# Kernel optimization log

Measured on AMD Instinct MI355X. Metric: run time of the kernel, lower is better.

The kernel has to match this reference:

```python
import jax, jax.numpy as jnp
import numpy as np

HEADS_FEAT = 8
HEADS_SAMP = 8
EPS = 1e-5


def _ln(x, g, b):
    m = jnp.mean(x, -1, keepdims=True)
    v = jnp.mean((x - m) ** 2, -1, keepdims=True)
    return (x - m) * jax.lax.rsqrt(v + EPS) * g + b


def _mha(q, k, v, heads, Wq, bq, Wk, bk, Wv, bv, Wo, bo, bias=None):
    # q: (N, Lq, D), k/v: (N, Lk, D); torch nn.MultiheadAttention math (eval, dropout=0)
    N, Lq, D = q.shape
    Lk = k.shape[1]
    dh = D // heads
    qh = (jnp.einsum('nld,ed->nle', q, Wq) + bq).reshape(N, Lq, heads, dh).transpose(0, 2, 1, 3)
    kh = (jnp.einsum('nld,ed->nle', k, Wk) + bk).reshape(N, Lk, heads, dh).transpose(0, 2, 1, 3)
    vh = (jnp.einsum('nld,ed->nle', v, Wv) + bv).reshape(N, Lk, heads, dh).transpose(0, 2, 1, 3)
    s = jnp.einsum('nhqd,nhkd->nhqk', qh, kh) * (dh ** -0.5)
    if bias is not None:
        s = s + bias  # bias broadcasts over heads
    a = jax.nn.softmax(s, axis=-1)
    o = jnp.einsum('nhqk,nhkd->nhqd', a, vh).transpose(0, 2, 1, 3).reshape(N, Lq, D)
    return jnp.einsum('nld,ed->nle', o, Wo) + bo


def setup_inputs() -> dict:
    key = jax.random.key(0)
    B, S, F, D = 4, 512, 32, 256
    H = 4 * D
    ks = iter(jax.random.split(key, 64))
    p = {}
    p['x'] = jax.random.normal(next(ks), (B, S, F, D), jnp.float32)
    m = jax.random.bernoulli(next(ks), 0.5, (B, F, F))
    p['attn_mask'] = m | jnp.eye(F, dtype=bool)  # diagonal True avoids fully-masked rows
    p['N_train'] = 384
    p['N_test'] = 128
    def W(shape):
        return jax.random.normal(next(ks), shape, jnp.float32) * 0.02
    for sfx in ('f', 't', 's'):
        for nm in ('Wq', 'Wk', 'Wv', 'Wo'):
            p[nm + '_' + sfx] = W((D, D))
        for nm in ('bq', 'bk', 'bv', 'bo'):
            p[nm + '_' + sfx] = jnp.zeros((D,), jnp.float32)
    for sfx in ('f', 't', 's', 'm'):
        p['g_' + sfx] = jnp.ones((D,), jnp.float32)
        p['b_' + sfx] = jnp.zeros((D,), jnp.float32)
    p['W1'] = W((H, D)); p['b1'] = jnp.zeros((H,), jnp.float32)
    p['Wg'] = W((H, D)); p['bg'] = jnp.zeros((H,), jnp.float32)
    p['W2'] = W((D, H)); p['b2'] = jnp.zeros((D,), jnp.float32)
    return p


def reference(x, attn_mask, N_train, N_test,
              Wq_f, bq_f, Wk_f, bk_f, Wv_f, bv_f, Wo_f, bo_f,
              Wq_t, bq_t, Wk_t, bk_t, Wv_t, bv_t, Wo_t, bo_t,
              Wq_s, bq_s, Wk_s, bk_s, Wv_s, bv_s, Wo_s, bo_s,
              g_f, b_f, g_t, b_t, g_s, b_s, g_m, b_m,
              W1, b1, Wg, bg, W2, b2):
    B, S, F, D = x.shape
    # --- graph-masked feature attention over F (rows = B*S) ---
    x_row = x.reshape(B * S, F, D)
    x_norm = _ln(x_row, g_f, b_f)
    bias = jnp.where(attn_mask, 0.0, -jnp.inf).astype(x.dtype)  # (B,F,F)
    bias = jnp.broadcast_to(bias[:, None, None], (B, S, 1, F, F)).reshape(B * S, 1, F, F)
    x2 = _mha(x_norm, x_norm, x_norm, HEADS_FEAT, Wq_f, bq_f, Wk_f, bk_f, Wv_f, bv_f, Wo_f, bo_f, bias)
    x_row = x_row + x2
    # --- sample attention over S (columns = B*F) ---
    x_col = x_row.reshape(B, S, F, D).transpose(0, 2, 1, 3).reshape(B * F, S, D)
    x_tr = x_col[:, :N_train]
    x_te = x_col[:, N_train:]
    x_trn = _ln(x_tr, g_t, b_t)
    x_tr = x_tr + _mha(x_trn, x_trn, x_trn, HEADS_SAMP, Wq_t, bq_t, Wk_t, bk_t, Wv_t, bv_t, Wo_t, bo_t)
    if N_test > 0:
        x_ten = _ln(x_te, g_s, b_s)
        kvn = _ln(x_tr, g_s, b_s)
        x_te = x_te + _mha(x_ten, kvn, kvn, HEADS_SAMP, Wq_s, bq_s, Wk_s, bk_s, Wv_s, bv_s, Wo_s, bo_s)
    xc = jnp.concatenate([x_tr, x_te], axis=1).reshape(B, F, S, D).transpose(0, 2, 1, 3)
    # --- SwiGLU MLP ---
    xn = _ln(xc, g_m, b_m)
    h = (jnp.einsum('bsfd,ed->bsfe', xn, W1) + b1) * jax.nn.silu(jnp.einsum('bsfd,ed->bsfe', xn, Wg) + bg)
    x2 = jnp.einsum('bsfe,de->bsfd', h, W2) + b2
    return xc + x2
```

## Files before the change

kernel.cpp:

```cpp
#include <hip/hip_runtime.h>

typedef unsigned short u16;
typedef __attribute__((ext_vector_type(8))) short short8;
typedef __attribute__((ext_vector_type(4))) float f32x4;

#define SCALE_QK 0.17677669529663687f
#define LOG2E 1.44269504088896f

__device__ __forceinline__ u16 f2b(float f) {
  union { float f; unsigned int i; } v; v.f = f;
  unsigned int x = v.i;
  x += 0x7fffu + ((x >> 16) & 1u);
  return (u16)(x >> 16);
}
__device__ __forceinline__ float lo16(unsigned int u) {
  union { unsigned int i; float f; } v; v.i = u << 16; return v.f;
}
__device__ __forceinline__ float hi16(unsigned int u) {
  union { unsigned int i; float f; } v; v.i = u & 0xffff0000u; return v.f;
}

__device__ __forceinline__ size_t map_off(int m, int map) {
  if (map == 0) return ((size_t)m) << 8;
  int r, s;
  if (map == 1) { r = m / 384; s = m - r * 384; }
  else          { r = m >> 7;  s = 384 + (m & 127); }
  int b = r >> 5, f = r & 31;
  return ((size_t)((b * 512 + s) * 32 + f)) << 8;
}

__global__ void decode_mask_kernel(const int* __restrict__ mraw,
                                   float* __restrict__ bias) {
  __shared__ int isbyte;
  if (threadIdx.x == 0) isbyte = 0;
  __syncthreads();
  for (int i = threadIdx.x; i < 1024; i += 256) {
    unsigned int v = (unsigned int)mraw[i];
    if (v > 1u) atomicOr(&isbyte, 1);
  }
  __syncthreads();
  bool byt = (isbyte != 0);
  const unsigned char* mb = (const unsigned char*)mraw;
  for (int i = threadIdx.x; i < 4096; i += 256) {
    bool on = byt ? (mb[i] != 0) : (mraw[i] != 0);
    bias[i] = on ? 0.f : -1e30f;
  }
}

struct WPtrs { const float* p[15]; };
__global__ __launch_bounds__(256) void cvt_w_kernel(WPtrs wp, u16* __restrict__ out) {
  int gid = blockIdx.x * 256 + threadIdx.x;
  int e0 = gid * 8;
  if (e0 >= 1572864) return;
  int mi, off;
  if (e0 < 786432) { mi = e0 >> 16; off = e0 & 65535; }
  else { int j = e0 - 786432; mi = 12 + (j >> 18); off = j & 262143; }
  const float* s = wp.p[mi] + off;
  float4 a = *(const float4*)s;
  float4 b = *(const float4*)(s + 4);
  union { u16 u[8]; uint4 v; } pk;
  pk.u[0] = f2b(a.x); pk.u[1] = f2b(a.y); pk.u[2] = f2b(a.z); pk.u[3] = f2b(a.w);
  pk.u[4] = f2b(b.x); pk.u[5] = f2b(b.y); pk.u[6] = f2b(b.z); pk.u[7] = f2b(b.w);
  *(uint4*)(out + e0) = pk.v;
}

__global__ __launch_bounds__(256) void ln_kernel(
    const float* __restrict__ src, float* __restrict__ cpy,
    u16* __restrict__ dst, const float* __restrict__ g,
    const float* __restrict__ bt, int M, int map) {
  int widx = blockIdx.x * 4 + (threadIdx.x >> 6);
  if (widx >= M) return;
  int lane = threadIdx.x & 63;
  size_t off = map_off(widx, map);
  float4 xv = ((const float4*)(src + off))[lane];
  float s = xv.x + xv.y + xv.z + xv.w;
#pragma unroll
  for (int o = 32; o; o >>= 1) s += __shfl_xor(s, o);
  float mean = s * (1.f / 256.f);
  float dx = xv.x - mean, dy = xv.y - mean, dz = xv.z - mean, dw = xv.w - mean;
  float ss = dx * dx + dy * dy + dz * dz + dw * dw;
#pragma unroll
  for (int o = 32; o; o >>= 1) ss += __shfl_xor(ss, o);
  float rs = rsqrtf(ss * (1.f / 256.f) + 1e-5f);
  float4 gv = ((const float4*)g)[lane];
  float4 bv = ((const float4*)bt)[lane];
  ushort4 st;
  st.x = f2b(dx * rs * gv.x + bv.x);
  st.y = f2b(dy * rs * gv.y + bv.y);
  st.z = f2b(dz * rs * gv.z + bv.z);
  st.w = f2b(dw * rs * gv.w + bv.w);
  *(ushort4*)(dst + ((size_t)widx << 8) + lane * 4) = st;
  if (cpy) ((float4*)(cpy + off))[lane] = xv;
}

__global__ __launch_bounds__(256) void gemm_nt(
    const u16* __restrict__ A, const u16* __restrict__ W,
    const float* __restrict__ bias, u16* __restrict__ outB,
    float* __restrict__ outF, int M, int N, int K, int mode) {
  __shared__ u16 As[2 * 64 * 32];
  __shared__ u16 Ws[2 * 64 * 32];
  int tid = threadIdx.x, lane = tid & 63, w = tid >> 6;
  int wr = w >> 1, wc = w & 1;
  int m0 = blockIdx.x * 64, n0 = blockIdx.y * 64;
  f32x4 z = {0.f, 0.f, 0.f, 0.f};
  f32x4 acc[2][2];
  acc[0][0] = z; acc[0][1] = z; acc[1][0] = z; acc[1][1] = z;
  int r = tid >> 2;
  int segbase = (tid & 3) << 1;
  for (int kt = 0; kt < K; kt += 64) {
#pragma unroll
    for (int c = 0; c < 2; ++c) {
      int seg = segbase + c;
      int dsti = (seg >> 2) * 2048 + r * 32 + (seg & 3) * 8;
      *(uint4*)&As[dsti] = *(const uint4*)(A + (size_t)(m0 + r) * K + kt + seg * 8);
      *(uint4*)&Ws[dsti] = *(const uint4*)(W + (size_t)(n0 + r) * K + kt + seg * 8);
    }
    __syncthreads();
#pragma unroll
    for (int ks = 0; ks < 2; ++ks) {
      const u16* ab = As + ks * 2048 + (lane & 15) * 32 + (lane >> 4) * 8;
      const u16* bb = Ws + ks * 2048 + (lane & 15) * 32 + (lane >> 4) * 8;
      short8 a0 = *(const short8*)(ab + (wr * 32) * 32);
      short8 a1 = *(const short8*)(ab + (wr * 32 + 16) * 32);
      short8 b0 = *(const short8*)(bb + (wc * 32) * 32);
      short8 b1 = *(const short8*)(bb + (wc * 32 + 16) * 32);
      acc[0][0] = __builtin_amdgcn_mfma_f32_16x16x32_bf16(a0, b0, acc[0][0], 0, 0, 0);
      acc[0][1] = __builtin_amdgcn_mfma_f32_16x16x32_bf16(a0, b1, acc[0][1], 0, 0, 0);
      acc[1][0] = __builtin_amdgcn_mfma_f32_16x16x32_bf16(a1, b0, acc[1][0], 0, 0, 0);
      acc[1][1] = __builtin_amdgcn_mfma_f32_16x16x32_bf16(a1, b1, acc[1][1], 0, 0, 0);
    }
    __syncthreads();
  }
  int ln_ = lane & 15, lg = lane >> 4;
#pragma unroll
  for (int mi = 0; mi < 2; ++mi)
#pragma unroll
    for (int ni = 0; ni < 2; ++ni) {
      int col = n0 + wc * 32 + ni * 16 + ln_;
      float bv = bias ? bias[col] : 0.f;
#pragma unroll
      for (int rr = 0; rr < 4; ++rr) {
        int row = m0 + wr * 32 + mi * 16 + lg * 4 + rr;
        float v = acc[mi][ni][rr] + bv;
        if (mode == 0) {
          outB[(size_t)row * N + col] = f2b(v);
        } else {
          size_t off = map_off(row, mode - 1) + col;
          outF[off] += v;
        }
      }
    }
}

__global__ __launch_bounds__(256) void gemm_dual(
    const u16* __restrict__ A, const u16* __restrict__ W1,
    const float* __restrict__ b1, const u16* __restrict__ Wg,
    const float* __restrict__ bg, u16* __restrict__ Hb,
    int M, int N, int K) {
  __shared__ u16 As[2 * 64 * 32];
  __shared__ u16 W1s[2 * 64 * 32];
  __shared__ u16 Wgs[2 * 64 * 32];
  int tid = threadIdx.x, lane = tid & 63, w = tid >> 6;
  int wr = w >> 1, wc = w & 1;
  int m0 = blockIdx.x * 64, n0 = blockIdx.y * 64;
  f32x4 z = {0.f, 0.f, 0.f, 0.f};
  f32x4 ac1[2][2], ac2[2][2];
  ac1[0][0] = z; ac1[0][1] = z; ac1[1][0] = z; ac1[1][1] = z;
  ac2[0][0] = z; ac2[0][1] = z; ac2[1][0] = z; ac2[1][1] = z;
  int r = tid >> 2;
  int segbase = (tid & 3) << 1;
  for (int kt = 0; kt < K; kt += 64) {
#pragma unroll
    for (int c = 0; c < 2; ++c) {
      int seg = segbase + c;
      int dsti = (seg >> 2) * 2048 + r * 32 + (seg & 3) * 8;
      *(uint4*)&As[dsti]  = *(const uint4*)(A  + (size_t)(m0 + r) * K + kt + seg * 8);
      *(uint4*)&W1s[dsti] = *(const uint4*)(W1 + (size_t)(n0 + r) * K + kt + seg * 8);
      *(uint4*)&Wgs[dsti] = *(const uint4*)(Wg + (size_t)(n0 + r) * K + kt + seg * 8);
    }
    __syncthreads();
#pragma unroll
    for (int ks = 0; ks < 2; ++ks) {
      const u16* ab = As + ks * 2048 + (lane & 15) * 32 + (lane >> 4) * 8;
      const u16* b1b = W1s + ks * 2048 + (lane & 15) * 32 + (lane >> 4) * 8;
      const u16* b2b = Wgs + ks * 2048 + (lane & 15) * 32 + (lane >> 4) * 8;
      short8 a0 = *(const short8*)(ab + (wr * 32) * 32);
      short8 a1 = *(const short8*)(ab + (wr * 32 + 16) * 32);
      short8 p0 = *(const short8*)(b1b + (wc * 32) * 32);
      short8 p1 = *(const short8*)(b1b + (wc * 32 + 16) * 32);
      short8 q0 = *(const short8*)(b2b + (wc * 32) * 32);
      short8 q1 = *(const short8*)(b2b + (wc * 32 + 16) * 32);
      ac1[0][0] = __builtin_amdgcn_mfma_f32_16x16x32_bf16(a0, p0, ac1[0][0], 0, 0, 0);
      ac1[0][1] = __builtin_amdgcn_mfma_f32_16x16x32_bf16(a0, p1, ac1[0][1], 0, 0, 0);
      ac1[1][0] = __builtin_amdgcn_mfma_f32_16x16x32_bf16(a1, p0, ac1[1][0], 0, 0, 0);
      ac1[1][1] = __builtin_amdgcn_mfma_f32_16x16x32_bf16(a1, p1, ac1[1][1], 0, 0, 0);
      ac2[0][0] = __builtin_amdgcn_mfma_f32_16x16x32_bf16(a0, q0, ac2[0][0], 0, 0, 0);
      ac2[0][1] = __builtin_amdgcn_mfma_f32_16x16x32_bf16(a0, q1, ac2[0][1], 0, 0, 0);
      ac2[1][0] = __builtin_amdgcn_mfma_f32_16x16x32_bf16(a1, q0, ac2[1][0], 0, 0, 0);
      ac2[1][1] = __builtin_amdgcn_mfma_f32_16x16x32_bf16(a1, q1, ac2[1][1], 0, 0, 0);
    }
    __syncthreads();
  }
  int ln_ = lane & 15, lg = lane >> 4;
#pragma unroll
  for (int mi = 0; mi < 2; ++mi)
#pragma unroll
    for (int ni = 0; ni < 2; ++ni) {
      int col = n0 + wc * 32 + ni * 16 + ln_;
      float bb1 = b1[col], bbg = bg[col];
#pragma unroll
      for (int rr = 0; rr < 4; ++rr) {
        int row = m0 + wr * 32 + mi * 16 + lg * 4 + rr;
        float v1 = ac1[mi][ni][rr] + bb1;
        float v2 = ac2[mi][ni][rr] + bbg;
        float sg = v2 / (1.f + __expf(-v2));
        Hb[(size_t)row * N + col] = f2b(v1 * sg);
      }
    }
}

__global__ __launch_bounds__(256) void fa_kernel(
    const u16* __restrict__ Q, const u16* __restrict__ K,
    const u16* __restrict__ V, u16* __restrict__ CTX,
    const float* __restrict__ bias) {
  __shared__ u16 Ks[8192];
  __shared__ u16 Vs[8192];
  __shared__ float Bs[1056];
  int tid = threadIdx.x;
  int row = blockIdx.x;
  size_t base = (size_t)row << 13;
#pragma unroll
  for (int it = 0; it < 4; ++it) {
    int c = it * 256 + tid;
    int tok = c >> 5, d8 = c & 31;
    int dst = ((d8 >> 2) * 32 + tok) * 32 + (d8 & 3) * 8;
    *(uint4*)&Ks[dst] = *(const uint4*)(K + base + tok * 256 + d8 * 8);
    *(uint4*)&Vs[dst] = *(const uint4*)(V + base + tok * 256 + d8 * 8);
  }
  {
    const float* bp = bias + (size_t)(row >> 9) * 1024;
#pragma unroll
    for (int it = 0; it < 4; ++it) {
      int i = it * 256 + tid;
      Bs[(i >> 5) * 33 + (i & 31)] = bp[i];
    }
  }
  __syncthreads();
  int h = tid >> 5, q = tid & 31;
  float qr[32];
  {
    const u16* qp = Q + base + q * 256 + h * 32;
    const float sc = SCALE_QK * LOG2E;
#pragma unroll
    for (int j = 0; j < 4; ++j) {
      uint4 u = ((const uint4*)qp)[j];
      qr[j * 8 + 0] = lo16(u.x) * sc; qr[j * 8 + 1] = hi16(u.x) * sc;
      qr[j * 8 + 2] = lo16(u.y) * sc; qr[j * 8 + 3] = hi16(u.y) * sc;
      qr[j * 8 + 4] = lo16(u.z) * sc; qr[j * 8 + 5] = hi16(u.z) * sc;
      qr[j * 8 + 6] = lo16(u.w) * sc; qr[j * 8 + 7] = hi16(u.w) * sc;
    }
  }
  float s[32], m = -3e38f;
  const u16* kb = Ks + h * 1024;
  const float* brow = Bs + q * 33;
#pragma unroll 4
  for (int k = 0; k < 32; ++k) {
    const uint4* kr = (const uint4*)(kb + k * 32);
    float d0 = 0.f, d1 = 0.f, d2 = 0.f, d3 = 0.f;
#pragma unroll
    for (int j = 0; j < 4; ++j) {
      uint4 u = kr[j];
      d0 += qr[j * 8 + 0] * lo16(u.x); d1 += qr[j * 8 + 1] * hi16(u.x);
      d2 += qr[j * 8 + 2] * lo16(u.y); d3 += qr[j * 8 + 3] * hi16(u.y);
      d0 += qr[j * 8 + 4] * lo16(u.z); d1 += qr[j * 8 + 5] * hi16(u.z);
      d2 += qr[j * 8 + 6] * lo16(u.w); d3 += qr[j * 8 + 7] * hi16(u.w);
    }
    float sv = (d0 + d1) + (d2 + d3) + brow[k];
    s[k] = sv;
    m = fmaxf(m, sv);
  }
  float l = 0.f;
#pragma unroll
  for (int k = 0; k < 32; ++k) {
    float p = exp2f(s[k] - m);
    s[k] = p; l += p;
  }
  float inv = 1.f / l;
  float out[32];
#pragma unroll
  for (int d = 0; d < 32; ++d) out[d] = 0.f;
  const u16* vb = Vs + h * 1024;
#pragma unroll 4
  for (int k = 0; k < 32; ++k) {
    float wgt = s[k];
    const uint4* vr = (const uint4*)(vb + k * 32);
#pragma unroll
    for (int j = 0; j < 4; ++j) {
      uint4 u = vr[j];
      out[j * 8 + 0] += wgt * lo16(u.x); out[j * 8 + 1] += wgt * hi16(u.x);
      out[j * 8 + 2] += wgt * lo16(u.y); out[j * 8 + 3] += wgt * hi16(u.y);
      out[j * 8 + 4] += wgt * lo16(u.z); out[j * 8 + 5] += wgt * hi16(u.z);
      out[j * 8 + 6] += wgt * lo16(u.w); out[j * 8 + 7] += wgt * hi16(u.w);
    }
  }
  u16* op = CTX + base + q * 256 + h * 32;
#pragma unroll
  for (int j = 0; j < 4; ++j) {
    union { u16 u[8]; uint4 v; } pk;
#pragma unroll
    for (int e = 0; e < 8; ++e) pk.u[e] = f2b(out[j * 8 + e] * inv);
    ((uint4*)op)[j] = pk.v;
  }
}

__global__ __launch_bounds__(256) void sa_mfma_kernel(
    const u16* __restrict__ Q, const u16* __restrict__ K,
    const u16* __restrict__ V, u16* __restrict__ CTX, int Lq) {
  __shared__ u16 Ks[384 * 40];
  __shared__ u16 Vt[32 * 392];
  __shared__ u16 Pb[4][16 * 72];
  int tid = threadIdx.x, lane = tid & 63, w = tid >> 6;
  int rh = blockIdx.x;
  int row = rh >> 3, h = rh & 7;
  size_t kvb = ((size_t)row * 384) * 256 + h * 32;
  for (int c = tid; c < 1536; c += 256) {
    int k = c >> 2, seg = c & 3;
    uint4 kk = *(const uint4*)(K + kvb + (size_t)k * 256 + seg * 8);
    *(uint4*)&Ks[k * 40 + seg * 8] = kk;
    uint4 vv = *(const uint4*)(V + kvb + (size_t)k * 256 + seg * 8);
    union { u16 u[8]; uint4 v; } t; t.v = vv;
#pragma unroll
    for (int j = 0; j < 8; ++j) Vt[(seg * 8 + j) * 392 + k] = t.u[j];
  }
  __syncthreads();
  int fr = lane & 15, fg = lane >> 4;
  const float sc = SCALE_QK * LOG2E;
  int nqt = Lq >> 4;
  f32x4 zz = {0.f, 0.f, 0.f, 0.f};
  for (int qt = w; qt < nqt; qt += 4) {
    int q0 = qt << 4;
    short8 a_q = *(const short8*)(Q + ((size_t)row * Lq + q0 + fr) * 256 + h * 32 + fg * 8);
    f32x4 O0 = zz, O1 = zz;
    float m[4] = {-3e38f, -3e38f, -3e38f, -3e38f};
    float l[4] = {0.f, 0.f, 0.f, 0.f};
    u16* pb = Pb[w];
    for (int c0 = 0; c0 < 384; c0 += 64) {
      f32x4 s[4];
#pragma unroll
      for (int kt = 0; kt < 4; ++kt) {
        short8 b_k = *(const short8*)(Ks + (c0 + kt * 16 + fr) * 40 + fg * 8);
        s[kt] = __builtin_amdgcn_mfma_f32_16x16x32_bf16(a_q, b_k, zz, 0, 0, 0);
      }
      float rm[4];
#pragma unroll
      for (int r = 0; r < 4; ++r)
        rm[r] = fmaxf(fmaxf(s[0][r], s[1][r]), fmaxf(s[2][r], s[3][r]));
#pragma unroll
      for (int o = 1; o <= 8; o <<= 1)
#pragma unroll
        for (int r = 0; r < 4; ++r) rm[r] = fmaxf(rm[r], __shfl_xor(rm[r], o));
      float al[4];
#pragma unroll
      for (int r = 0; r < 4; ++r) {
        float mn = fmaxf(m[r], rm[r] * sc);
        al[r] = exp2f(m[r] - mn);
        m[r] = mn;
        l[r] *= al[r];
        O0[r] *= al[r];
        O1[r] *= al[r];
      }
#pragma unroll
      for (int kt = 0; kt < 4; ++kt)
#pragma unroll
        for (int r = 0; r < 4; ++r) {
          float p = exp2f(fmaf(s[kt][r], sc, -m[r]));
          l[r] += p;
          pb[(fg * 4 + r) * 72 + kt * 16 + fr] = f2b(p);
        }
      asm volatile("s_waitcnt lgkmcnt(0)" ::: "memory");
      __builtin_amdgcn_wave_barrier();
#pragma unroll
      for (int sub = 0; sub < 2; ++sub) {
        short8 a_p = *(const short8*)(pb + fr * 72 + sub * 32 + fg * 8);
        short8 b_v0 = *(const short8*)(Vt + fr * 392 + c0 + sub * 32 + fg * 8);
        short8 b_v1 = *(const short8*)(Vt + (16 + fr) * 392 + c0 + sub * 32 + fg * 8);
        O0 = __builtin_amdgcn_mfma_f32_16x16x32_bf16(a_p, b_v0, O0, 0, 0, 0);
        O1 = __builtin_amdgcn_mfma_f32_16x16x32_bf16(a_p, b_v1, O1, 0, 0, 0);
      }
      __builtin_amdgcn_wave_barrier();
    }
#pragma unroll
    for (int o = 1; o <= 8; o <<= 1)
#pragma unroll
      for (int r = 0; r < 4; ++r) l[r] += __shfl_xor(l[r], o);
    u16* op = CTX + ((size_t)row * Lq + q0) * 256 + h * 32;
#pragma unroll
    for (int r = 0; r < 4; ++r) {
      float inv = 1.f / l[r];
      int orow = fg * 4 + r;
      op[orow * 256 + fr] = f2b(O0[r] * inv);
      op[orow * 256 + 16 + fr] = f2b(O1[r] * inv);
    }
  }
}

extern "C" void kernel_launch(void* const* d_in, const int* in_sizes, int n_in,
                              void* d_out, int out_size, void* d_ws, size_t ws_size,
                              hipStream_t stream) {
  const float* x    = (const float*)d_in[0];
  const int*   mask = (const int*)d_in[1];
  const float* bq_f = (const float*)d_in[8],  *bk_f = (const float*)d_in[9];
  const float* bv_f = (const float*)d_in[10], *bo_f = (const float*)d_in[11];
  const float* bq_t = (const float*)d_in[16], *bk_t = (const float*)d_in[17];
  const float* bv_t = (const float*)d_in[18], *bo_t = (const float*)d_in[19];
  const float* bq_s = (const float*)d_in[24], *bk_s = (const float*)d_in[25];
  const float* bv_s = (const float*)d_in[26], *bo_s = (const float*)d_in[27];
  const float* g_f = (const float*)d_in[28], *b_f = (const float*)d_in[29];
  const float* g_t = (const float*)d_in[30], *b_t = (const float*)d_in[31];
  const float* g_s = (const float*)d_in[32], *b_s = (const float*)d_in[33];
  const float* g_m = (const float*)d_in[34], *b_m = (const float*)d_in[35];
  const float* b1 = (const float*)d_in[37];
  const float* bg = (const float*)d_in[39];
  const float* b2 = (const float*)d_in[41];

  float* XR = (float*)d_out;
  char* ws = (char*)d_ws;
  float* BIAS = (float*)ws;
  u16* XN = (u16*)(ws + 16384);
  u16* QB = XN + 16777216;
  u16* KB = QB + 16777216;
  u16* VB = KB + 16777216;
  u16* XM = VB + 16777216;
  u16* WB = XM + 16777216;
  u16* HB = XN;

  WPtrs wp;
  wp.p[0] = (const float*)d_in[4];  wp.p[1] = (const float*)d_in[5];
  wp.p[2] = (const float*)d_in[6];  wp.p[3] = (const float*)d_in[7];
  wp.p[4] = (const float*)d_in[12]; wp.p[5] = (const float*)d_in[13];
  wp.p[6] = (const float*)d_in[14]; wp.p[7] = (const float*)d_in[15];
  wp.p[8] = (const float*)d_in[20]; wp.p[9] = (const float*)d_in[21];
  wp.p[10] = (const float*)d_in[22]; wp.p[11] = (const float*)d_in[23];
  wp.p[12] = (const float*)d_in[36]; wp.p[13] = (const float*)d_in[38];
  wp.p[14] = (const float*)d_in[40];
  const u16 *WQF = WB, *WKF = WB + 65536, *WVF = WB + 131072, *WOF = WB + 196608;
  const u16 *WQT = WB + 262144, *WKT = WB + 327680, *WVT = WB + 393216, *WOT = WB + 458752;
  const u16 *WQS = WB + 524288, *WKS = WB + 589824, *WVS = WB + 655360, *WOS = WB + 720896;
  const u16 *W1B = WB + 786432, *WGB = WB + 1048576, *W2B = WB + 1310720;

  cvt_w_kernel<<<768, 256, 0, stream>>>(wp, WB);
  decode_mask_kernel<<<1, 256, 0, stream>>>(mask, BIAS);

  ln_kernel<<<16384, 256, 0, stream>>>(x, XR, XN, g_f, b_f, 65536, 0);
  gemm_nt<<<dim3(1024, 4), 256, 0, stream>>>(XN, WQF, bq_f, QB, nullptr, 65536, 256, 256, 0);
  gemm_nt<<<dim3(1024, 4), 256, 0, stream>>>(XN, WKF, bk_f, KB, nullptr, 65536, 256, 256, 0);
  gemm_nt<<<dim3(1024, 4), 256, 0, stream>>>(XN, WVF, bv_f, VB, nullptr, 65536, 256, 256, 0);
  fa_kernel<<<2048, 256, 0, stream>>>(QB, KB, VB, XN, BIAS);
  gemm_nt<<<dim3(1024, 4), 256, 0, stream>>>(XN, WOF, bo_f, nullptr, XR, 65536, 256, 256, 1);

  ln_kernel<<<12288, 256, 0, stream>>>(XR, nullptr, XN, g_t, b_t, 49152, 1);
  gemm_nt<<<dim3(768, 4), 256, 0, stream>>>(XN, WQT, bq_t, QB, nullptr, 49152, 256, 256, 0);
  gemm_nt<<<dim3(768, 4), 256, 0, stream>>>(XN, WKT, bk_t, KB, nullptr, 49152, 256, 256, 0);
  gemm_nt<<<dim3(768, 4), 256, 0, stream>>>(XN, WVT, bv_t, VB, nullptr, 49152, 256, 256, 0);
  sa_mfma_kernel<<<1024, 256, 0, stream>>>(QB, KB, VB, XN, 384);
  gemm_nt<<<dim3(768, 4), 256, 0, stream>>>(XN, WOT, bo_t, nullptr, XR, 49152, 256, 256, 2);

  ln_kernel<<<4096, 256, 0, stream>>>(XR, nullptr, XN, g_s, b_s, 16384, 2);
  gemm_nt<<<dim3(256, 4), 256, 0, stream>>>(XN, WQS, bq_s, QB, nullptr, 16384, 256, 256, 0);
  ln_kernel<<<12288, 256, 0, stream>>>(XR, nullptr, XN, g_s, b_s, 49152, 1);
  gemm_nt<<<dim3(768, 4), 256, 0, stream>>>(XN, WKS, bk_s, KB, nullptr, 49152, 256, 256, 0);
  gemm_nt<<<dim3(768, 4), 256, 0, stream>>>(XN, WVS, bv_s, VB, nullptr, 49152, 256, 256, 0);
  sa_mfma_kernel<<<1024, 256, 0, stream>>>(QB, KB, VB, XN, 128);
  gemm_nt<<<dim3(256, 4), 256, 0, stream>>>(XN, WOS, bo_s, nullptr, XR, 16384, 256, 256, 3);

  ln_kernel<<<16384, 256, 0, stream>>>(XR, nullptr, XM, g_m, b_m, 65536, 0);
  gemm_dual<<<dim3(1024, 16), 256, 0, stream>>>(XM, W1B, b1, WGB, bg, HB, 65536, 1024, 256);
  gemm_nt<<<dim3(1024, 4), 256, 0, stream>>>(HB, W2B, b2, nullptr, XR, 65536, 256, 1024, 1);
}
```

Before: 975.7 us.

## Enlarge GEMM tiles to 128x128 and load tiles via direct global-to-LDS

Both GEMM kernels move from 64x64 to 128x128 output tiles with a 4x4 MFMA accumulator grid per wave, which raises operand reuse out of LDS and cuts redundant global reads. Tile staging now uses global_load_lds to copy straight into shared memory instead of going through registers. The catch is much higher register pressure, especially in gemm_dual with 32 accumulators, and unpadded 64-wide LDS rows that may cause bank conflicts. Launch grids are halved in each dimension to match.

```diff
diff --git a/kernel.cpp b/kernel.cpp
--- a/kernel.cpp
+++ b/kernel.cpp
@@ -18,6 +18,11 @@
 }
 __device__ __forceinline__ float hi16(unsigned int u) {
   union { unsigned int i; float f; } v; v.i = u & 0xffff0000u; return v.f;
+}
+__device__ __forceinline__ void gll16(const void* g, void* l) {
+  __builtin_amdgcn_global_load_lds(
+      (const __attribute__((address_space(1))) unsigned int*)g,
+      (__attribute__((address_space(3))) unsigned int*)l, 16, 0, 0);
 }
 
 __device__ __forceinline__ size_t map_off(int m, int map) {
@@ -93,126 +98,132 @@
   if (cpy) ((float4*)(cpy + off))[lane] = xv;
 }
 
-__global__ __launch_bounds__(256) void gemm_nt(
+__global__ __launch_bounds__(256, 2) void gemm_nt(
     const u16* __restrict__ A, const u16* __restrict__ W,
     const float* __restrict__ bias, u16* __restrict__ outB,
     float* __restrict__ outF, int M, int N, int K, int mode) {
-  __shared__ u16 As[2 * 64 * 32];
-  __shared__ u16 Ws[2 * 64 * 32];
+  __shared__ u16 As[128 * 64];
+  __shared__ u16 Bs[128 * 64];
   int tid = threadIdx.x, lane = tid & 63, w = tid >> 6;
   int wr = w >> 1, wc = w & 1;
-  int m0 = blockIdx.x * 64, n0 = blockIdx.y * 64;
+  int m0 = blockIdx.x * 128, n0 = blockIdx.y * 128;
+  int fr = lane & 15, fg = lane >> 4;
   f32x4 z = {0.f, 0.f, 0.f, 0.f};
-  f32x4 acc[2][2];
-  acc[0][0] = z; acc[0][1] = z; acc[1][0] = z; acc[1][1] = z;
-  int r = tid >> 2;
-  int segbase = (tid & 3) << 1;
+  f32x4 acc[4][4];
+#pragma unroll
+  for (int i = 0; i < 4; ++i)
+#pragma unroll
+    for (int j = 0; j < 4; ++j) acc[i][j] = z;
+  int r8 = lane >> 3, seg = lane & 7;
+  const u16* gA = A + (size_t)(m0 + w * 32 + r8) * K + seg * 8;
+  const u16* gB = W + (size_t)(n0 + w * 32 + r8) * K + seg * 8;
+  u16* lA = As + (w * 32) * 64;
+  u16* lB = Bs + (w * 32) * 64;
   for (int kt = 0; kt < K; kt += 64) {
 #pragma unroll
-    for (int c = 0; c < 2; ++c) {
-      int seg = segbase + c;
-      int dsti = (seg >> 2) * 2048 + r * 32 + (seg & 3) * 8;
-      *(uint4*)&As[dsti] = *(const uint4*)(A + (size_t)(m0 + r) * K + kt + seg * 8);
-      *(uint4*)&Ws[dsti] = *(const uint4*)(W + (size_t)(n0 + r) * K + kt + seg * 8);
+    for (int j = 0; j < 4; ++j) {
+      gll16(gA + (size_t)(j * 8) * K + kt, lA + j * 512);
+      gll16(gB + (size_t)(j * 8) * K + kt, lB + j * 512);
     }
     __syncthreads();
 #pragma unroll
     for (int ks = 0; ks < 2; ++ks) {
-      const u16* ab = As + ks * 2048 + (lane & 15) * 32 + (lane >> 4) * 8;
-      const u16* bb = Ws + ks * 2048 + (lane & 15) * 32 + (lane >> 4) * 8;
-      short8 a0 = *(const short8*)(ab + (wr * 32) * 32);
-      short8 a1 = *(const short8*)(ab + (wr * 32 + 16) * 32);
-      short8 b0 = *(const short8*)(bb + (wc * 32) * 32);
-      short8 b1 = *(const short8*)(bb + (wc * 32 + 16) * 32);
-      acc[0][0] = __builtin_amdgcn_mfma_f32_16x16x32_bf16(a0, b0, acc[0][0], 0, 0, 0);
-      acc[0][1] = __builtin_amdgcn_mfma_f32_16x16x32_bf16(a0, b1, acc[0][1], 0, 0, 0);
-      acc[1][0] = __builtin_amdgcn_mfma_f32_16x16x32_bf16(a1, b0, acc[1][0], 0, 0, 0);
-      acc[1][1] = __builtin_amdgcn_mfma_f32_16x16x32_bf16(a1, b1, acc[1][1], 0, 0, 0);
+      short8 af[4], bf[4];
+#pragma unroll
+      for (int i = 0; i < 4; ++i) {
+        af[i] = *(const short8*)(As + (wr * 64 + i * 16 + fr) * 64 + ks * 32 + fg * 8);
+        bf[i] = *(const short8*)(Bs + (wc * 64 + i * 16 + fr) * 64 + ks * 32 + fg * 8);
+      }
+#pragma unroll
+      for (int mi = 0; mi < 4; ++mi)
+#pragma unroll
+        for (int ni = 0; ni < 4; ++ni)
+          acc[mi][ni] = __builtin_amdgcn_mfma_f32_16x16x32_bf16(af[mi], bf[ni], acc[mi][ni], 0, 0, 0);
     }
     __syncthreads();
   }
-  int ln_ = lane & 15, lg = lane >> 4;
-#pragma unroll
-  for (int mi = 0; mi < 2; ++mi)
-#pragma unroll
-    for (int ni = 0; ni < 2; ++ni) {
-      int col = n0 + wc * 32 + ni * 16 + ln_;
+#pragma unroll
+  for (int mi = 0; mi < 4; ++mi)
+#pragma unroll
+    for (int ni = 0; ni < 4; ++ni) {
+      int col = n0 + wc * 64 + ni * 16 + fr;
       float bv = bias ? bias[col] : 0.f;
 #pragma unroll
-      for (int rr = 0; rr < 4; ++rr) {
-        int row = m0 + wr * 32 + mi * 16 + lg * 4 + rr;
-        float v = acc[mi][ni][rr] + bv;
+      for (int r = 0; r < 4; ++r) {
+        int row = m0 + wr * 64 + mi * 16 + fg * 4 + r;
+        float v = acc[mi][ni][r] + bv;
         if (mode == 0) {
           outB[(size_t)row * N + col] = f2b(v);
         } else {
-          size_t off = map_off(row, mode - 1) + col;
-          outF[off] += v;
+          outF[map_off(row, mode - 1) + col] += v;
         }
       }
     }
 }
 
-__global__ __launch_bounds__(256) void gemm_dual(
+__global__ __launch_bounds__(256, 2) void gemm_dual(
     const u16* __restrict__ A, const u16* __restrict__ W1,
     const float* __restrict__ b1, const u16* __restrict__ Wg,
     const float* __restrict__ bg, u16* __restrict__ Hb,
     int M, int N, int K) {
-  __shared__ u16 As[2 * 64 * 32];
-  __shared__ u16 W1s[2 * 64 * 32];
-  __shared__ u16 Wgs[2 * 64 * 32];
+  __shared__ u16 As[128 * 64];
+  __shared__ u16 W1s[128 * 64];
+  __shared__ u16 Wgs[128 * 64];
   int tid = threadIdx.x, lane = tid & 63, w = tid >> 6;
   int wr = w >> 1, wc = w & 1;
-  int m0 = blockIdx.x * 64, n0 = blockIdx.y * 64;
+  int m0 = blockIdx.x * 128, n0 = blockIdx.y * 128;
+  int fr = lane & 15, fg = lane >> 4;
   f32x4 z = {0.f, 0.f, 0.f, 0.f};
-  f32x4 ac1[2][2], ac2[2][2];
-  ac1[0][0] = z; ac1[0][1] = z; ac1[1][0] = z; ac1[1][1] = z;
-  ac2[0][0] = z; ac2[0][1] = z; ac2[1][0] = z; ac2[1][1] = z;
-  int r = tid >> 2;
-  int segbase = (tid & 3) << 1;
+  f32x4 ac1[4][4], ac2[4][4];
+#pragma unroll
+  for (int i = 0; i < 4; ++i)
+#pragma unroll
+    for (int j = 0; j < 4; ++j) { ac1[i][j] = z; ac2[i][j] = z; }
+  int r8 = lane >> 3, seg = lane & 7;
+  const u16* gA = A + (size_t)(m0 + w * 32 + r8) * K + seg * 8;
+  const u16* g1 = W1 + (size_t)(n0 + w * 32 + r8) * K + seg * 8;
+  const u16* g2 = Wg + (size_t)(n0 + w * 32 + r8) * K + seg * 8;
+  u16* lA = As + (w * 32) * 64;
+  u16* l1 = W1s + (w * 32) * 64;
+  u16* l2 = Wgs + (w * 32) * 64;
   for (int kt = 0; kt < K; kt += 64) {
 #pragma unroll
-    for (int c = 0; c < 2; ++c) {
-      int seg = segbase + c;
-      int dsti = (seg >> 2) * 2048 + r * 32 + (seg & 3) * 8;
-      *(uint4*)&As[dsti]  = *(const uint4*)(A  + (size_t)(m0 + r) * K + kt + seg * 8);
-      *(uint4*)&W1s[dsti] = *(const uint4*)(W1 + (size_t)(n0 + r) * K + kt + seg * 8);
-      *(uint4*)&Wgs[dsti] = *(const uint4*)(Wg + (size_t)(n0 + r) * K + kt + seg * 8);
+    for (int j = 0; j < 4; ++j) {
+      gll16(gA + (size_t)(j * 8) * K + kt, lA + j * 512);
+      gll16(g1 + (size_t)(j * 8) * K + kt, l1 + j * 512);
+      gll16(g2 + (size_t)(j * 8) * K + kt, l2 + j * 512);
     }
     __syncthreads();
 #pragma unroll
     for (int ks = 0; ks < 2; ++ks) {
-      const u16* ab = As + ks * 2048 + (lane & 15) * 32 + (lane >> 4) * 8;
-      const u16* b1b = W1s + ks * 2048 + (lane & 15) * 32 + (lane >> 4) * 8;
-      const u16* b2b = Wgs + ks * 2048 + (lane & 15) * 32 + (lane >> 4) * 8;
-      short8 a0 = *(const short8*)(ab + (wr * 32) * 32);
-      short8 a1 = *(const short8*)(ab + (wr * 32 + 16) * 32);
-      short8 p0 = *(const short8*)(b1b + (wc * 32) * 32);
-      short8 p1 = *(const short8*)(b1b + (wc * 32 + 16) * 32);
-      short8 q0 = *(const short8*)(b2b + (wc * 32) * 32);
-      short8 q1 = *(const short8*)(b2b + (wc * 32 + 16) * 32);
-      ac1[0][0] = __builtin_amdgcn_mfma_f32_16x16x32_bf16(a0, p0, ac1[0][0], 0, 0, 0);
-      ac1[0][1] = __builtin_amdgcn_mfma_f32_16x16x32_bf16(a0, p1, ac1[0][1], 0, 0, 0);
-      ac1[1][0] = __builtin_amdgcn_mfma_f32_16x16x32_bf16(a1, p0, ac1[1][0], 0, 0, 0);
-      ac1[1][1] = __builtin_amdgcn_mfma_f32_16x16x32_bf16(a1, p1, ac1[1][1], 0, 0, 0);
-      ac2[0][0] = __builtin_amdgcn_mfma_f32_16x16x32_bf16(a0, q0, ac2[0][0], 0, 0, 0);
-      ac2[0][1] = __builtin_amdgcn_mfma_f32_16x16x32_bf16(a0, q1, ac2[0][1], 0, 0, 0);
-      ac2[1][0] = __builtin_amdgcn_mfma_f32_16x16x32_bf16(a1, q0, ac2[1][0], 0, 0, 0);
-      ac2[1][1] = __builtin_amdgcn_mfma_f32_16x16x32_bf16(a1, q1, ac2[1][1], 0, 0, 0);
+      short8 af[4], bf1[4], bf2[4];
+#pragma unroll
+      for (int i = 0; i < 4; ++i) {
+        af[i]  = *(const short8*)(As  + (wr * 64 + i * 16 + fr) * 64 + ks * 32 + fg * 8);
+        bf1[i] = *(const short8*)(W1s + (wc * 64 + i * 16 + fr) * 64 + ks * 32 + fg * 8);
+        bf2[i] = *(const short8*)(Wgs + (wc * 64 + i * 16 + fr) * 64 + ks * 32 + fg * 8);
+      }
+#pragma unroll
+      for (int mi = 0; mi < 4; ++mi)
+#pragma unroll
+        for (int ni = 0; ni < 4; ++ni) {
+          ac1[mi][ni] = __builtin_amdgcn_mfma_f32_16x16x32_bf16(af[mi], bf1[ni], ac1[mi][ni], 0, 0, 0);
+          ac2[mi][ni] = __builtin_amdgcn_mfma_f32_16x16x32_bf16(af[mi], bf2[ni], ac2[mi][ni], 0, 0, 0);
+        }
     }
     __syncthreads();
   }
-  int ln_ = lane & 15, lg = lane >> 4;
-#pragma unroll
-  for (int mi = 0; mi < 2; ++mi)
-#pragma unroll
-    for (int ni = 0; ni < 2; ++ni) {
-      int col = n0 + wc * 32 + ni * 16 + ln_;
+#pragma unroll
+  for (int mi = 0; mi < 4; ++mi)
+#pragma unroll
+    for (int ni = 0; ni < 4; ++ni) {
+      int col = n0 + wc * 64 + ni * 16 + fr;
       float bb1 = b1[col], bbg = bg[col];
 #pragma unroll
-      for (int rr = 0; rr < 4; ++rr) {
-        int row = m0 + wr * 32 + mi * 16 + lg * 4 + rr;
-        float v1 = ac1[mi][ni][rr] + bb1;
-        float v2 = ac2[mi][ni][rr] + bbg;
+      for (int r = 0; r < 4; ++r) {
+        int row = m0 + wr * 64 + mi * 16 + fg * 4 + r;
+        float v1 = ac1[mi][ni][r] + bb1;
+        float v2 = ac2[mi][ni][r] + bbg;
         float sg = v2 / (1.f + __expf(-v2));
         Hb[(size_t)row * N + col] = f2b(v1 * sg);
       }
@@ -452,28 +463,28 @@
   decode_mask_kernel<<<1, 256, 0, stream>>>(mask, BIAS);
 
   ln_kernel<<<16384, 256, 0, stream>>>(x, XR, XN, g_f, b_f, 65536, 0);
-  gemm_nt<<<dim3(1024, 4), 256, 0, stream>>>(XN, WQF, bq_f, QB, nullptr, 65536, 256, 256, 0);
-  gemm_nt<<<dim3(1024, 4), 256, 0, stream>>>(XN, WKF, bk_f, KB, nullptr, 65536, 256, 256, 0);
-  gemm_nt<<<dim3(1024, 4), 256, 0, stream>>>(XN, WVF, bv_f, VB, nullptr, 65536, 256, 256, 0);
+  gemm_nt<<<dim3(512, 2), 256, 0, stream>>>(XN, WQF, bq_f, QB, nullptr, 65536, 256, 256, 0);
+  gemm_nt<<<dim3(512, 2), 256, 0, stream>>>(XN, WKF, bk_f, KB, nullptr, 65536, 256, 256, 0);
+  gemm_nt<<<dim3(512, 2), 256, 0, stream>>>(XN, WVF, bv_f, VB, nullptr, 65536, 256, 256, 0);
   fa_kernel<<<2048, 256, 0, stream>>>(QB, KB, VB, XN, BIAS);
-  gemm_nt<<<dim3(1024, 4), 256, 0, stream>>>(XN, WOF, bo_f, nullptr, XR, 65536, 256, 256, 1);
+  gemm_nt<<<dim3(512, 2), 256, 0, stream>>>(XN, WOF, bo_f, nullptr, XR, 65536, 256, 256, 1);
 
   ln_kernel<<<12288, 256, 0, stream>>>(XR, nullptr, XN, g_t, b_t, 49152, 1);
-  gemm_nt<<<dim3(768, 4), 256, 0, stream>>>(XN, WQT, bq_t, QB, nullptr, 49152, 256, 256, 0);
-  gemm_nt<<<dim3(768, 4), 256, 0, stream>>>(XN, WKT, bk_t, KB, nullptr, 49152, 256, 256, 0);
-  gemm_nt<<<dim3(768, 4), 256, 0, stream>>>(XN, WVT, bv_t, VB, nullptr, 49152, 256, 256, 0);
+  gemm_nt<<<dim3(384, 2), 256, 0, stream>>>(XN, WQT, bq_t, QB, nullptr, 49152, 256, 256, 0);
+  gemm_nt<<<dim3(384, 2), 256, 0, stream>>>(XN, WKT, bk_t, KB, nullptr, 49152, 256, 256, 0);
+  gemm_nt<<<dim3(384, 2), 256, 0, stream>>>(XN, WVT, bv_t, VB, nullptr, 49152, 256, 256, 0);
   sa_mfma_kernel<<<1024, 256, 0, stream>>>(QB, KB, VB, XN, 384);
-  gemm_nt<<<dim3(768, 4), 256, 0, stream>>>(XN, WOT, bo_t, nullptr, XR, 49152, 256, 256, 2);
+  gemm_nt<<<dim3(384, 2), 256, 0, stream>>>(XN, WOT, bo_t, nullptr, XR, 49152, 256, 256, 2);
 
   ln_kernel<<<4096, 256, 0, stream>>>(XR, nullptr, XN, g_s, b_s, 16384, 2);
-  gemm_nt<<<dim3(256, 4), 256, 0, stream>>>(XN, WQS, bq_s, QB, nullptr, 16384, 256, 256, 0);
+  gemm_nt<<<dim3(128, 2), 256, 0, stream>>>(XN, WQS, bq_s, QB, nullptr, 16384, 256, 256, 0);
   ln_kernel<<<12288, 256, 0, stream>>>(XR, nullptr, XN, g_s, b_s, 49152, 1);
-  gemm_nt<<<dim3(768, 4), 256, 0, stream>>>(XN, WKS, bk_s, KB, nullptr, 49152, 256, 256, 0);
-  gemm_nt<<<dim3(768, 4), 256, 0, stream>>>(XN, WVS, bv_s, VB, nullptr, 49152, 256, 256, 0);
+  gemm_nt<<<dim3(384, 2), 256, 0, stream>>>(XN, WKS, bk_s, KB, nullptr, 49152, 256, 256, 0);
+  gemm_nt<<<dim3(384, 2), 256, 0, stream>>>(XN, WVS, bv_s, VB, nullptr, 49152, 256, 256, 0);
   sa_mfma_kernel<<<1024, 256, 0, stream>>>(QB, KB, VB, XN, 128);
-  gemm_nt<<<dim3(256, 4), 256, 0, stream>>>(XN, WOS, bo_s, nullptr, XR, 16384, 256, 256, 3);
+  gemm_nt<<<dim3(128, 2), 256, 0, stream>>>(XN, WOS, bo_s, nullptr, XR, 16384, 256, 256, 3);
 
   ln_kernel<<<16384, 256, 0, stream>>>(XR, nullptr, XM, g_m, b_m, 65536, 0);
-  gemm_dual<<<dim3(1024, 16), 256, 0, stream>>>(XM, W1B, b1, WGB, bg, HB, 65536, 1024, 256);
-  gemm_nt<<<dim3(1024, 4), 256, 0, stream>>>(HB, W2B, b2, nullptr, XR, 65536, 256, 1024, 1);
-}
+  gemm_dual<<<dim3(512, 8), 256, 0, stream>>>(XM, W1B, b1, WGB, bg, HB, 65536, 1024, 256);
+  gemm_nt<<<dim3(512, 2), 256, 0, stream>>>(HB, W2B, b2, nullptr, XR, 65536, 256, 1024, 1);
+}
```

Result: slower. 1.063 ms (+9.0%).
